# Optimization experiments

Hardware: AMD Instinct MI355X
Metric: run time of the kernel (lower is better)

Reference implementation:

```python
import jax, jax.numpy as jnp
import numpy as np

DIM = 2048   # token width; == heads*head_dim
H, DH = 16, 128
B, S = 1, 2048
E, K = 4, 2          # routed experts, top-k
HID = 5632           # per-expert SwiGLU hidden: round256(int(2*(4*DIM)/3))
HS = 2816            # shared expert hidden: round256(int(2*(2*DIM)/3))


def setup_inputs() -> dict:
    key = jax.random.key(0)
    ks = jax.random.split(key, 24)
    def g(i, shape, s=0.02):
        return jax.random.normal(ks[i], shape, dtype=jnp.float32) * s
    return {
        "image_tokens": jax.random.normal(ks[0], (B, S, DIM), dtype=jnp.float32),
        "adaln_input": jax.random.normal(ks[1], (B, DIM), dtype=jnp.float32),
        "W_ada": g(2, (DIM, 6 * DIM)), "b_ada": g(3, (6 * DIM,)),
        "Wq": g(4, (DIM, DIM)), "bq": g(5, (DIM,)),
        "Wk": g(6, (DIM, DIM)), "bk": g(7, (DIM,)),
        "Wv": g(8, (DIM, DIM)), "bv": g(9, (DIM,)),
        "q_rms_w": jnp.ones((DIM,), jnp.float32) + g(10, (DIM,)),
        "k_rms_w": jnp.ones((DIM,), jnp.float32) + g(11, (DIM,)),
        "Wo": g(12, (DIM, DIM)), "bo": g(13, (DIM,)),
        "gate_w": g(14, (E, DIM)),
        "We1": g(15, (E, DIM, HID)), "We3": g(16, (E, DIM, HID)), "We2": g(17, (E, HID, DIM)),
        "Ws1": g(18, (DIM, HS)), "Ws3": g(19, (DIM, HS)), "Ws2": g(20, (HS, DIM)),
    }


def _ln(x):  # LayerNorm, elementwise_affine=False, eps=1e-6
    m = jnp.mean(x, -1, keepdims=True)
    v = jnp.var(x, -1, keepdims=True)
    return (x - m) * jax.lax.rsqrt(v + 1e-6)


def _rms(x, w):  # RMSNorm with affine weight, eps=1e-5
    return x * jax.lax.rsqrt(jnp.mean(x * x, -1, keepdims=True) + 1e-5) * w


def reference(image_tokens, adaln_input, W_ada, b_ada, Wq, bq, Wk, bk, Wv, bv,
              q_rms_w, k_rms_w, Wo, bo, gate_w, We1, We3, We2, Ws1, Ws3, Ws2):
    # adaLN: SiLU -> Linear -> 6 chunks, each broadcast as [B,1,dim]
    mod = (jax.nn.silu(adaln_input) @ W_ada + b_ada)[:, None, :]
    sh_msa, sc_msa, g_msa, sh_mlp, sc_mlp, g_mlp = jnp.split(mod, 6, axis=-1)

    # attention branch
    x = _ln(image_tokens) * (1.0 + sc_msa) + sh_msa
    q = _rms(x @ Wq + bq, q_rms_w).reshape(B, S, H, DH)
    k = _rms(x @ Wk + bk, k_rms_w).reshape(B, S, H, DH)
    v = (x @ Wv + bv).reshape(B, S, H, DH)
    att = jax.nn.softmax(jnp.einsum('bihd,bjhd->bhij', q, k) / jnp.sqrt(jnp.float32(DH)), axis=-1)
    o = jnp.einsum('bhij,bjhd->bihd', att, v).reshape(B, S, DIM) @ Wo + bo
    img = g_msa * o + image_tokens

    # MoE SwiGLU FFN branch
    y = _ln(img) * (1.0 + sc_mlp) + sh_mlp
    xf = y.reshape(-1, DIM)                                   # [N, dim]
    scores = jax.nn.softmax(xf @ gate_w.T, axis=-1)           # [N, E]
    tw, ti = jax.lax.top_k(scores, K)                         # no top-k renorm (norm_topk_prob=False)
    comb = jnp.zeros((xf.shape[0], E), xf.dtype).at[jnp.arange(xf.shape[0])[:, None], ti].add(tw)
    h = jax.nn.silu(jnp.einsum('nd,edh->neh', xf, We1)) * jnp.einsum('nd,edh->neh', xf, We3)
    routed = jnp.einsum('neh,ehd,ne->nd', h, We2, comb)
    shared = (jax.nn.silu(xf @ Ws1) * (xf @ Ws3)) @ Ws2
    ff = (routed + shared).reshape(B, S, DIM)

    return g_mlp * ff + img
```

## Files before the change

kernel.cpp:

```cpp
#include <hip/hip_runtime.h>
#include <hip/hip_bf16.h>

typedef unsigned short u16;
typedef __bf16 bf16x8 __attribute__((ext_vector_type(8)));
typedef float f32x4 __attribute__((ext_vector_type(4)));
typedef unsigned short u16x8 __attribute__((ext_vector_type(8)));

constexpr int DIMC = 2048;
constexpr int SEQ = 2048;
constexpr int NHEAD = 16;
constexpr int HDIM = 128;
constexpr int NEXP = 4;
constexpr int HIDC = 5632;
constexpr int HSH = 2816;
constexpr int MOD6 = 6 * DIMC;
constexpr int RSTRIDE = 2304;

static __device__ __forceinline__ u16 f2bf(float f) {
  __hip_bfloat16 b = __float2bfloat16(f);
  return __builtin_bit_cast(u16, b);
}
static __device__ __forceinline__ float bf2f(u16 u) {
  unsigned int x = ((unsigned int)u) << 16;
  return __builtin_bit_cast(float, x);
}
static __device__ __forceinline__ float sigf(float x) { return 1.f / (1.f + __expf(-x)); }
static __device__ __forceinline__ void splitf(float f, u16& h, u16& l) {
  h = f2bf(f);
  l = f2bf(f - bf2f(h));
}

static __device__ __forceinline__ void gload16(const void* src, void* dst) {
  __builtin_amdgcn_global_load_lds((const __attribute__((address_space(1))) void*)src,
                                   (__attribute__((address_space(3))) void*)dst, 16, 0, 0);
}

static __device__ __forceinline__ float blockSum(float v) {
#pragma unroll
  for (int m = 1; m < 64; m <<= 1) v += __shfl_xor(v, m);
  __shared__ float s[4];
  int w = threadIdx.x >> 6;
  if ((threadIdx.x & 63) == 0) s[w] = v;
  __syncthreads();
  float r = s[0] + s[1] + s[2] + s[3];
  __syncthreads();
  return r;
}

__global__ __launch_bounds__(256) void k_transpose(const float* __restrict__ in, u16* __restrict__ out,
                                                   int R, int C, int ldin, size_t inz, size_t outz) {
  __shared__ __align__(16) float tile[32][33];
  const float* inp = in + (size_t)blockIdx.z * inz;
  u16* outp = out + (size_t)blockIdx.z * outz;
  int tx = threadIdx.x & 31, ty = threadIdx.x >> 5;
  int c0 = blockIdx.x * 32, r0 = blockIdx.y * 32;
#pragma unroll
  for (int i = 0; i < 32; i += 8)
    tile[ty + i][tx] = inp[(size_t)(r0 + ty + i) * ldin + c0 + tx];
  __syncthreads();
#pragma unroll
  for (int i = 0; i < 32; i += 8)
    outp[(size_t)(c0 + ty + i) * R + r0 + tx] = f2bf(tile[tx][ty + i]);
}

__global__ __launch_bounds__(256) void k_transpose_s(const float* __restrict__ in, u16* __restrict__ outh,
                                                     u16* __restrict__ outl, int R, int C, int ldin) {
  __shared__ __align__(16) float tile[32][33];
  int tx = threadIdx.x & 31, ty = threadIdx.x >> 5;
  int c0 = blockIdx.x * 32, r0 = blockIdx.y * 32;
#pragma unroll
  for (int i = 0; i < 32; i += 8)
    tile[ty + i][tx] = in[(size_t)(r0 + ty + i) * ldin + c0 + tx];
  __syncthreads();
#pragma unroll
  for (int i = 0; i < 32; i += 8) {
    float v = tile[tx][ty + i];
    u16 h, l;
    splitf(v, h, l);
    size_t idx = (size_t)(c0 + ty + i) * R + r0 + tx;
    outh[idx] = h;
    outl[idx] = l;
  }
}

__global__ __launch_bounds__(256) void k_adaln_p(const float* __restrict__ a, const float* __restrict__ W,
                                                 float* __restrict__ partial) {
  __shared__ float sa[128];
  int tid = threadIdx.x, slice = blockIdx.y;
  if (tid < 128) { float v = a[slice * 128 + tid]; sa[tid] = v * sigf(v); }
  __syncthreads();
  int j = blockIdx.x * 256 + tid;
  float acc = 0.f;
#pragma unroll 4
  for (int d = 0; d < 128; ++d) acc += sa[d] * W[(size_t)(slice * 128 + d) * MOD6 + j];
  partial[(size_t)slice * MOD6 + j] = acc;
}
__global__ __launch_bounds__(256) void k_adaln_r(const float* __restrict__ partial, const float* __restrict__ b,
                                                 float* __restrict__ mod) {
  int j = blockIdx.x * 256 + threadIdx.x;
  float acc = b[j];
#pragma unroll
  for (int s = 0; s < 16; ++s) acc += partial[(size_t)s * MOD6 + j];
  mod[j] = acc;
}

__global__ __launch_bounds__(256) void k_ln_mod_split(const float* __restrict__ X, const float* __restrict__ mod,
                                                      int shOff, int scOff, u16* __restrict__ outh,
                                                      u16* __restrict__ outl) {
  int row = blockIdx.x, tid = threadIdx.x;
  const float4* x4 = (const float4*)(X + (size_t)row * DIMC);
  float4 v0 = x4[tid * 2], v1 = x4[tid * 2 + 1];
  float s = v0.x + v0.y + v0.z + v0.w + v1.x + v1.y + v1.z + v1.w;
  float ss = v0.x * v0.x + v0.y * v0.y + v0.z * v0.z + v0.w * v0.w +
             v1.x * v1.x + v1.y * v1.y + v1.z * v1.z + v1.w * v1.w;
  s = blockSum(s);
  ss = blockSum(ss);
  float mean = s * (1.f / DIMC);
  float var = ss * (1.f / DIMC) - mean * mean;
  float rstd = rsqrtf(var + 1e-6f);
  const float* sh = mod + shOff;
  const float* sc = mod + scOff;
  int c = tid * 8;
  float xv[8] = {v0.x, v0.y, v0.z, v0.w, v1.x, v1.y, v1.z, v1.w};
  u16x8 oh, ol;
#pragma unroll
  for (int e = 0; e < 8; ++e) {
    float v = (xv[e] - mean) * rstd * (1.f + sc[c + e]) + sh[c + e];
    u16 h, l;
    splitf(v, h, l);
    oh[e] = h;
    ol[e] = l;
  }
  *(u16x8*)(outh + (size_t)row * DIMC + c) = oh;
  *(u16x8*)(outl + (size_t)row * DIMC + c) = ol;
}

__global__ __launch_bounds__(256) void k_ln_mod(const float* __restrict__ X, const float* __restrict__ mod,
                                                int shOff, int scOff, u16* __restrict__ out) {
  int row = blockIdx.x, tid = threadIdx.x;
  const float4* x4 = (const float4*)(X + (size_t)row * DIMC);
  float4 v0 = x4[tid * 2], v1 = x4[tid * 2 + 1];
  float s = v0.x + v0.y + v0.z + v0.w + v1.x + v1.y + v1.z + v1.w;
  float ss = v0.x * v0.x + v0.y * v0.y + v0.z * v0.z + v0.w * v0.w +
             v1.x * v1.x + v1.y * v1.y + v1.z * v1.z + v1.w * v1.w;
  s = blockSum(s);
  ss = blockSum(ss);
  float mean = s * (1.f / DIMC);
  float var = ss * (1.f / DIMC) - mean * mean;
  float rstd = rsqrtf(var + 1e-6f);
  const float* sh = mod + shOff;
  const float* sc = mod + scOff;
  int c = tid * 8;
  float xv[8] = {v0.x, v0.y, v0.z, v0.w, v1.x, v1.y, v1.z, v1.w};
  u16x8 o;
#pragma unroll
  for (int e = 0; e < 8; ++e) o[e] = f2bf((xv[e] - mean) * rstd * (1.f + sc[c + e]) + sh[c + e]);
  *(u16x8*)(out + (size_t)row * DIMC + c) = o;
}

__global__ __launch_bounds__(256) void k_rms_split(const float* __restrict__ X, int ldin,
                                                   const float* __restrict__ w, float scale,
                                                   u16* __restrict__ outh, u16* __restrict__ outl) {
  int row = blockIdx.x, tid = threadIdx.x;
  const float4* x4 = (const float4*)(X + (size_t)row * ldin);
  float4 v0 = x4[tid * 2], v1 = x4[tid * 2 + 1];
  float ss = v0.x * v0.x + v0.y * v0.y + v0.z * v0.z + v0.w * v0.w +
             v1.x * v1.x + v1.y * v1.y + v1.z * v1.z + v1.w * v1.w;
  ss = blockSum(ss);
  float rstd = rsqrtf(ss * (1.f / DIMC) + 1e-5f) * scale;
  int c = tid * 8;
  float xv[8] = {v0.x, v0.y, v0.z, v0.w, v1.x, v1.y, v1.z, v1.w};
  u16x8 oh, ol;
#pragma unroll
  for (int e = 0; e < 8; ++e) {
    float v = xv[e] * rstd * w[c + e];
    u16 h, l;
    splitf(v, h, l);
    oh[e] = h;
    ol[e] = l;
  }
  *(u16x8*)(outh + (size_t)row * DIMC + c) = oh;
  *(u16x8*)(outl + (size_t)row * DIMC + c) = ol;
}

__global__ __launch_bounds__(256) void k_gate(const float* __restrict__ img, const float* __restrict__ mod,
                                              const float* __restrict__ gw, float* __restrict__ comb) {
  int n = blockIdx.x, tid = threadIdx.x;
  const float4* x4 = (const float4*)(img + (size_t)n * DIMC);
  float4 v0 = x4[tid * 2], v1 = x4[tid * 2 + 1];
  float s = v0.x + v0.y + v0.z + v0.w + v1.x + v1.y + v1.z + v1.w;
  float ss = v0.x * v0.x + v0.y * v0.y + v0.z * v0.z + v0.w * v0.w +
             v1.x * v1.x + v1.y * v1.y + v1.z * v1.z + v1.w * v1.w;
  s = blockSum(s);
  ss = blockSum(ss);
  float mean = s * (1.f / DIMC);
  float var = ss * (1.f / DIMC) - mean * mean;
  float rstd = rsqrtf(var + 1e-6f);
  const float* sh = mod + 3 * DIMC;
  const float* sc = mod + 4 * DIMC;
  int c = tid * 8;
  float xv[8] = {v0.x, v0.y, v0.z, v0.w, v1.x, v1.y, v1.z, v1.w};
  float y[8];
#pragma unroll
  for (int e = 0; e < 8; ++e) y[e] = (xv[e] - mean) * rstd * (1.f + sc[c + e]) + sh[c + e];
  float accs[NEXP];
#pragma unroll
  for (int ex = 0; ex < NEXP; ++ex) {
    float a = 0.f;
#pragma unroll
    for (int e = 0; e < 8; ++e) a += y[e] * gw[(size_t)ex * DIMC + c + e];
    accs[ex] = blockSum(a);
  }
  if (tid == 0) {
    float mx = fmaxf(fmaxf(accs[0], accs[1]), fmaxf(accs[2], accs[3]));
    float ex0 = __expf(accs[0] - mx), ex1 = __expf(accs[1] - mx);
    float ex2 = __expf(accs[2] - mx), ex3 = __expf(accs[3] - mx);
    float inv = 1.f / (ex0 + ex1 + ex2 + ex3);
    float v[4] = {ex0 * inv, ex1 * inv, ex2 * inv, ex3 * inv};
    int i1 = 0;
    for (int e = 1; e < 4; ++e)
      if (v[e] > v[i1]) i1 = e;
    int i2 = -1;
    for (int e = 0; e < 4; ++e) {
      if (e == i1) continue;
      if (i2 < 0 || v[e] > v[i2]) i2 = e;
    }
    for (int e = 0; e < 4; ++e) comb[(size_t)n * 4 + e] = (e == i1 || e == i2) ? v[e] : 0.f;
  }
}

__global__ __launch_bounds__(256) void k_route(const float* __restrict__ comb, int* __restrict__ gidx,
                                               float* __restrict__ cw, int* __restrict__ Mpad) {
  int wid = threadIdx.x >> 6, lane = threadIdx.x & 63;
  int base = 0;
  for (int c = 0; c < SEQ; c += 64) {
    int n = c + lane;
    float w = comb[(size_t)n * NEXP + wid];
    bool sel = w > 0.f;
    unsigned long long mask = __ballot(sel);
    int pos = __popcll(mask & ((1ull << lane) - 1ull));
    if (sel) {
      gidx[wid * RSTRIDE + base + pos] = n;
      cw[wid * RSTRIDE + base + pos] = w;
    }
    base += __popcll(mask);
  }
  int padded = (base + 127) & ~127;
  for (int i = base + lane; i < padded; i += 64) {
    gidx[wid * RSTRIDE + i] = -1;
    cw[wid * RSTRIDE + i] = 0.f;
  }
  if (lane == 0) Mpad[wid] = padded;
}

__global__ __launch_bounds__(256, 2) void k_gemmD(const u16* __restrict__ A, const u16* __restrict__ BT,
                                                  int M, int N, int K, float* __restrict__ Cf) {
  __shared__ __align__(16) u16 As[2][8192], Bs[2][8192];
  const int tid = threadIdx.x, wid = tid >> 6, lane = tid & 63;
  const int l16 = lane & 15, g = lane >> 4;
  const int wr = wid >> 1, wc = wid & 1;
  const int m0 = blockIdx.y * 128, n0 = blockIdx.x * 128;
  const int srow = lane >> 2, scol = (lane & 3) * 8;
  const u16* aS0 = A + (size_t)(m0 + wid * 32 + srow) * K + scol;
  const u16* aS1 = aS0 + (size_t)16 * K;
  const u16* bS0 = BT + (size_t)(n0 + wid * 32 + srow) * K + scol;
  const u16* bS1 = bS0 + (size_t)16 * K;

  const f32x4 zero4 = {0.f, 0.f, 0.f, 0.f};
  f32x4 acc[4][4];
#pragma unroll
  for (int mi = 0; mi < 4; ++mi)
#pragma unroll
    for (int ni = 0; ni < 4; ++ni) acc[mi][ni] = zero4;

  auto stage = [&](int b, int k0) {
    gload16(aS0 + k0, &As[b][wid * 1024]);
    gload16(aS1 + k0, &As[b][wid * 1024 + 512]);
    gload16(aS0 + k0 + 32, &As[b][4096 + wid * 1024]);
    gload16(aS1 + k0 + 32, &As[b][4096 + wid * 1024 + 512]);
    gload16(bS0 + k0, &Bs[b][wid * 1024]);
    gload16(bS1 + k0, &Bs[b][wid * 1024 + 512]);
    gload16(bS0 + k0 + 32, &Bs[b][4096 + wid * 1024]);
    gload16(bS1 + k0 + 32, &Bs[b][4096 + wid * 1024 + 512]);
  };
  auto compute = [&](int b) {
#pragma unroll
    for (int hh = 0; hh < 2; ++hh) {
      const u16* Asrc = &As[b][hh * 4096];
      const u16* Bsrc = &Bs[b][hh * 4096];
      bf16x8 af[4], bfr[4];
#pragma unroll
      for (int mi = 0; mi < 4; ++mi)
        af[mi] = *(const bf16x8*)(&Asrc[(wr * 64 + mi * 16 + l16) * 32 + g * 8]);
#pragma unroll
      for (int ni = 0; ni < 4; ++ni)
        bfr[ni] = *(const bf16x8*)(&Bsrc[(wc * 64 + ni * 16 + l16) * 32 + g * 8]);
#pragma unroll
      for (int mi = 0; mi < 4; ++mi)
#pragma unroll
        for (int ni = 0; ni < 4; ++ni)
          acc[mi][ni] = __builtin_amdgcn_mfma_f32_16x16x32_bf16(af[mi], bfr[ni], acc[mi][ni], 0, 0, 0);
    }
  };

  stage(0, 0);
  __syncthreads();
  for (int k0 = 0; k0 < K; k0 += 128) {
    if (k0 + 64 < K) stage(1, k0 + 64);
    compute(0);
    __syncthreads();
    if (k0 + 128 < K) stage(0, k0 + 128);
    compute(1);
    __syncthreads();
  }

#pragma unroll
  for (int mi = 0; mi < 4; ++mi)
#pragma unroll
    for (int ni = 0; ni < 4; ++ni) {
      const int col = n0 + wc * 64 + ni * 16 + l16;
#pragma unroll
      for (int r = 0; r < 4; ++r) {
        const int row = m0 + wr * 64 + mi * 16 + g * 4 + r;
        Cf[(size_t)row * N + col] = acc[mi][ni][r];
      }
    }
}

template <int GATH>
__global__ __launch_bounds__(256, 2) void k_gemmUP(const u16* __restrict__ A, const u16* __restrict__ B1T0,
                                                   const u16* __restrict__ B3T0, size_t bz, int N, int K,
                                                   const int* __restrict__ gidx0,
                                                   const float* __restrict__ cw0,
                                                   const int* __restrict__ Mp0, u16* __restrict__ G0,
                                                   size_t cz) {
  const int z = blockIdx.z;
  const int m0 = blockIdx.y * 128;
  const int* gidxE = nullptr;
  const float* cwE = nullptr;
  if constexpr (GATH) {
    if (m0 >= Mp0[z]) return;
    gidxE = gidx0 + (size_t)z * RSTRIDE;
    cwE = cw0 + (size_t)z * RSTRIDE;
  }
  const u16* B1T = B1T0 + (size_t)z * bz;
  const u16* B3T = B3T0 + (size_t)z * bz;
  u16* G = G0 + (size_t)z * cz;

  __shared__ __align__(16) u16 As[8192], B1s[8192], B3s[8192];
  const int tid = threadIdx.x, wid = tid >> 6, lane = tid & 63;
  const int l16 = lane & 15, g = lane >> 4;
  const int wr = wid >> 1, wc = wid & 1;
  const int n0 = blockIdx.x * 128;
  const int srow = lane >> 2, scol = (lane & 3) * 8;
  const int slot0 = m0 + wid * 32 + srow;
  int row0, row1;
  if constexpr (GATH) {
    int t0 = gidxE[slot0], t1 = gidxE[slot0 + 16];
    row0 = t0 < 0 ? 0 : t0;
    row1 = t1 < 0 ? 0 : t1;
  } else {
    row0 = slot0;
    row1 = slot0 + 16;
  }
  const u16* aS0 = A + (size_t)row0 * K + scol;
  const u16* aS1 = A + (size_t)row1 * K + scol;
  const u16* b1S0 = B1T + (size_t)(n0 + wid * 32 + srow) * K + scol;
  const u16* b1S1 = b1S0 + (size_t)16 * K;
  const u16* b3S0 = B3T + (size_t)(n0 + wid * 32 + srow) * K + scol;
  const u16* b3S1 = b3S0 + (size_t)16 * K;

  const f32x4 zero4 = {0.f, 0.f, 0.f, 0.f};
  f32x4 acc1[4][4], acc3[4][4];
#pragma unroll
  for (int mi = 0; mi < 4; ++mi)
#pragma unroll
    for (int ni = 0; ni < 4; ++ni) {
      acc1[mi][ni] = zero4;
      acc3[mi][ni] = zero4;
    }

  for (int k0 = 0; k0 < K; k0 += 64) {
    __syncthreads();
    gload16(aS0 + k0, &As[wid * 1024]);
    gload16(aS1 + k0, &As[wid * 1024 + 512]);
    gload16(aS0 + k0 + 32, &As[4096 + wid * 1024]);
    gload16(aS1 + k0 + 32, &As[4096 + wid * 1024 + 512]);
    gload16(b1S0 + k0, &B1s[wid * 1024]);
    gload16(b1S1 + k0, &B1s[wid * 1024 + 512]);
    gload16(b1S0 + k0 + 32, &B1s[4096 + wid * 1024]);
    gload16(b1S1 + k0 + 32, &B1s[4096 + wid * 1024 + 512]);
    gload16(b3S0 + k0, &B3s[wid * 1024]);
    gload16(b3S1 + k0, &B3s[wid * 1024 + 512]);
    gload16(b3S0 + k0 + 32, &B3s[4096 + wid * 1024]);
    gload16(b3S1 + k0 + 32, &B3s[4096 + wid * 1024 + 512]);
    __syncthreads();
#pragma unroll
    for (int hh = 0; hh < 2; ++hh) {
      const u16* Asrc = &As[hh * 4096];
      const u16* B1src = &B1s[hh * 4096];
      const u16* B3src = &B3s[hh * 4096];
      bf16x8 af[4], b1f[4], b3f[4];
#pragma unroll
      for (int mi = 0; mi < 4; ++mi)
        af[mi] = *(const bf16x8*)(&Asrc[(wr * 64 + mi * 16 + l16) * 32 + g * 8]);
#pragma unroll
      for (int ni = 0; ni < 4; ++ni) {
        b1f[ni] = *(const bf16x8*)(&B1src[(wc * 64 + ni * 16 + l16) * 32 + g * 8]);
        b3f[ni] = *(const bf16x8*)(&B3src[(wc * 64 + ni * 16 + l16) * 32 + g * 8]);
      }
#pragma unroll
      for (int mi = 0; mi < 4; ++mi)
#pragma unroll
        for (int ni = 0; ni < 4; ++ni) {
          acc1[mi][ni] = __builtin_amdgcn_mfma_f32_16x16x32_bf16(af[mi], b1f[ni], acc1[mi][ni], 0, 0, 0);
          acc3[mi][ni] = __builtin_amdgcn_mfma_f32_16x16x32_bf16(af[mi], b3f[ni], acc3[mi][ni], 0, 0, 0);
        }
    }
  }

#pragma unroll
  for (int mi = 0; mi < 4; ++mi)
#pragma unroll
    for (int ni = 0; ni < 4; ++ni) {
      const int col = n0 + wc * 64 + ni * 16 + l16;
#pragma unroll
      for (int r = 0; r < 4; ++r) {
        const int slot = m0 + wr * 64 + mi * 16 + g * 4 + r;
        float hv = bf2f(f2bf(acc1[mi][ni][r]));
        float sw = hv * sigf(hv);
        float val = sw * acc3[mi][ni][r];
        if constexpr (GATH) val = val * cwE[slot];
        G[(size_t)slot * N + col] = f2bf(val);
      }
    }
}

__global__ __launch_bounds__(256, 2) void k_gemmR2(const u16* __restrict__ A, const u16* __restrict__ BT,
                                                   int N, int K, const int* __restrict__ gidxE,
                                                   const int* __restrict__ MpE, float* __restrict__ ff) {
  const int m0 = blockIdx.y * 128;
  if (m0 >= *MpE) return;
  __shared__ __align__(16) u16 As[2][8192], Bs[2][8192];
  const int tid = threadIdx.x, wid = tid >> 6, lane = tid & 63;
  const int l16 = lane & 15, g = lane >> 4;
  const int wr = wid >> 1, wc = wid & 1;
  const int n0 = blockIdx.x * 128;
  const int srow = lane >> 2, scol = (lane & 3) * 8;
  const int slot0 = m0 + wid * 32 + srow;
  const u16* aS0 = A + (size_t)slot0 * K + scol;
  const u16* aS1 = A + (size_t)(slot0 + 16) * K + scol;
  const u16* bS0 = BT + (size_t)(n0 + wid * 32 + srow) * K + scol;
  const u16* bS1 = bS0 + (size_t)16 * K;

  const f32x4 zero4 = {0.f, 0.f, 0.f, 0.f};
  f32x4 acc[4][4];
#pragma unroll
  for (int mi = 0; mi < 4; ++mi)
#pragma unroll
    for (int ni = 0; ni < 4; ++ni) acc[mi][ni] = zero4;

  auto stage = [&](int b, int k0) {
    gload16(aS0 + k0, &As[b][wid * 1024]);
    gload16(aS1 + k0, &As[b][wid * 1024 + 512]);
    gload16(aS0 + k0 + 32, &As[b][4096 + wid * 1024]);
    gload16(aS1 + k0 + 32, &As[b][4096 + wid * 1024 + 512]);
    gload16(bS0 + k0, &Bs[b][wid * 1024]);
    gload16(bS1 + k0, &Bs[b][wid * 1024 + 512]);
    gload16(bS0 + k0 + 32, &Bs[b][4096 + wid * 1024]);
    gload16(bS1 + k0 + 32, &Bs[b][4096 + wid * 1024 + 512]);
  };
  auto compute = [&](int b) {
#pragma unroll
    for (int hh = 0; hh < 2; ++hh) {
      const u16* Asrc = &As[b][hh * 4096];
      const u16* Bsrc = &Bs[b][hh * 4096];
      bf16x8 af[4], bfr[4];
#pragma unroll
      for (int mi = 0; mi < 4; ++mi)
        af[mi] = *(const bf16x8*)(&Asrc[(wr * 64 + mi * 16 + l16) * 32 + g * 8]);
#pragma unroll
      for (int ni = 0; ni < 4; ++ni)
        bfr[ni] = *(const bf16x8*)(&Bsrc[(wc * 64 + ni * 16 + l16) * 32 + g * 8]);
#pragma unroll
      for (int mi = 0; mi < 4; ++mi)
#pragma unroll
        for (int ni = 0; ni < 4; ++ni)
          acc[mi][ni] = __builtin_amdgcn_mfma_f32_16x16x32_bf16(af[mi], bfr[ni], acc[mi][ni], 0, 0, 0);
    }
  };

  stage(0, 0);
  __syncthreads();
  for (int k0 = 0; k0 < K; k0 += 128) {
    if (k0 + 64 < K) stage(1, k0 + 64);
    compute(0);
    __syncthreads();
    if (k0 + 128 < K) stage(0, k0 + 128);
    compute(1);
    __syncthreads();
  }

#pragma unroll
  for (int mi = 0; mi < 4; ++mi)
#pragma unroll
    for (int ni = 0; ni < 4; ++ni) {
      const int col = n0 + wc * 64 + ni * 16 + l16;
#pragma unroll
      for (int r = 0; r < 4; ++r) {
        const int slot = m0 + wr * 64 + mi * 16 + g * 4 + r;
        int t = gidxE[slot];
        if (t >= 0) ff[(size_t)t * N + col] += acc[mi][ni][r];
      }
    }
}

template <int MODE>
__global__ __launch_bounds__(256, 2) void k_gemm3s(const u16* __restrict__ Ahg, const u16* __restrict__ Alg,
                                                   const u16* __restrict__ Bhg, const u16* __restrict__ Blg,
                                                   int M, int N, int K, float* __restrict__ Cf,
                                                   const float* __restrict__ bias0,
                                                   const float* __restrict__ bias1,
                                                   const float* __restrict__ bias2,
                                                   const float* __restrict__ gvec,
                                                   const float* __restrict__ resid) {
  __shared__ __align__(16) u16 Ahs[2][4096], Als[2][4096], Bhs[2][4096], Bls[2][4096];
  const int tid = threadIdx.x, wid = tid >> 6, lane = tid & 63;
  const int l16 = lane & 15, g = lane >> 4;
  const int wr = wid >> 1, wc = wid & 1;
  const int m0 = blockIdx.y * 128, n0 = blockIdx.x * 128;
  const int srow = lane >> 2, scol = (lane & 3) * 8;
  const size_t aOff0 = (size_t)(m0 + wid * 32 + srow) * K + scol;
  const size_t aOff1 = aOff0 + (size_t)16 * K;
  const size_t bOff0 = (size_t)(n0 + wid * 32 + srow) * K + scol;
  const size_t bOff1 = bOff0 + (size_t)16 * K;

  const f32x4 zero4 = {0.f, 0.f, 0.f, 0.f};
  f32x4 acc[4][4];
#pragma unroll
  for (int mi = 0; mi < 4; ++mi)
#pragma unroll
    for (int ni = 0; ni < 4; ++ni) acc[mi][ni] = zero4;

  auto stage = [&](int b, int k0) {
    gload16(Ahg + aOff0 + k0, &Ahs[b][wid * 1024]);
    gload16(Ahg + aOff1 + k0, &Ahs[b][wid * 1024 + 512]);
    gload16(Alg + aOff0 + k0, &Als[b][wid * 1024]);
    gload16(Alg + aOff1 + k0, &Als[b][wid * 1024 + 512]);
    gload16(Bhg + bOff0 + k0, &Bhs[b][wid * 1024]);
    gload16(Bhg + bOff1 + k0, &Bhs[b][wid * 1024 + 512]);
    gload16(Blg + bOff0 + k0, &Bls[b][wid * 1024]);
    gload16(Blg + bOff1 + k0, &Bls[b][wid * 1024 + 512]);
  };
  auto compute = [&](int b) {
    bf16x8 bhf[4], blf[4];
#pragma unroll
    for (int ni = 0; ni < 4; ++ni) {
      bhf[ni] = *(const bf16x8*)(&Bhs[b][(wc * 64 + ni * 16 + l16) * 32 + g * 8]);
      blf[ni] = *(const bf16x8*)(&Bls[b][(wc * 64 + ni * 16 + l16) * 32 + g * 8]);
    }
#pragma unroll
    for (int mi = 0; mi < 4; ++mi) {
      bf16x8 ahf = *(const bf16x8*)(&Ahs[b][(wr * 64 + mi * 16 + l16) * 32 + g * 8]);
      bf16x8 alf = *(const bf16x8*)(&Als[b][(wr * 64 + mi * 16 + l16) * 32 + g * 8]);
#pragma unroll
      for (int ni = 0; ni < 4; ++ni) {
        acc[mi][ni] = __builtin_amdgcn_mfma_f32_16x16x32_bf16(alf, bhf[ni], acc[mi][ni], 0, 0, 0);
        acc[mi][ni] = __builtin_amdgcn_mfma_f32_16x16x32_bf16(ahf, blf[ni], acc[mi][ni], 0, 0, 0);
        acc[mi][ni] = __builtin_amdgcn_mfma_f32_16x16x32_bf16(ahf, bhf[ni], acc[mi][ni], 0, 0, 0);
      }
    }
  };

  stage(0, 0);
  __syncthreads();
  for (int k0 = 0; k0 < K; k0 += 64) {
    if (k0 + 32 < K) stage(1, k0 + 32);
    compute(0);
    __syncthreads();
    if (k0 + 64 < K) stage(0, k0 + 64);
    compute(1);
    __syncthreads();
  }

  const float* bp = bias0;
  if constexpr (MODE == 7) bp = (n0 < DIMC) ? bias0 : (n0 < 2 * DIMC ? bias1 : bias2);
#pragma unroll
  for (int mi = 0; mi < 4; ++mi)
#pragma unroll
    for (int ni = 0; ni < 4; ++ni) {
      const int col = n0 + wc * 64 + ni * 16 + l16;
      float bv = bp ? bp[col & (DIMC - 1)] : 0.f;
#pragma unroll
      for (int r = 0; r < 4; ++r) {
        const int row = m0 + wr * 64 + mi * 16 + g * 4 + r;
        float v = acc[mi][ni][r] + bv;
        if constexpr (MODE == 7) {
          Cf[(size_t)row * N + col] = v;
        } else {
          Cf[(size_t)row * N + col] = v * gvec[col] + resid[(size_t)row * N + col];
        }
      }
    }
}

__global__ __launch_bounds__(256, 3) void k_flash3(const u16* __restrict__ qh_g, const u16* __restrict__ ql_g,
                                                   const u16* __restrict__ kh_g, const u16* __restrict__ kl_g,
                                                   const u16* __restrict__ vth_g, const u16* __restrict__ vtl_g,
                                                   u16* __restrict__ oh_g, u16* __restrict__ ol_g) {
  __shared__ __align__(16) u16 Kh[4096], Kl[4096], Vh[128 * 40], Vl[128 * 40];
  __shared__ __align__(16) u16 Pah[4][16 * 40], Pal[4][16 * 40];
  const int tid = threadIdx.x, wid = tid >> 6, lane = tid & 63;
  const int l16 = lane & 15, g = lane >> 4;
  const int h = blockIdx.y;
  const int r0 = blockIdx.x * 64 + wid * 16;
  const size_t hOff = (size_t)h * HDIM;

  bf16x8 qfh[4], qfl[4];
#pragma unroll
  for (int kc = 0; kc < 4; ++kc) {
    const size_t qo = (size_t)(r0 + l16) * DIMC + hOff + kc * 32 + g * 8;
    qfh[kc] = *(const bf16x8*)(qh_g + qo);
    qfl[kc] = *(const bf16x8*)(ql_g + qo);
  }

  const int kr = tid >> 3, ke0 = (tid & 7) * 16;
  const int kswz = (kr & 7) << 4;
  const int kc0 = (ke0 * 2) ^ kswz, kc1 = (ke0 * 2 + 16) ^ kswz;
  char* khp = (char*)Kh + kr * 256;
  char* klp = (char*)Kl + kr * 256;
  const size_t kOff = (size_t)kr * DIMC + hOff + ke0;
  const int vr = tid >> 1, ve0 = (tid & 1) * 16;
  char* vhp = (char*)Vh + vr * 80 + ve0 * 2;
  char* vlp = (char*)Vl + vr * 80 + ve0 * 2;
  const size_t vOff = (size_t)(hOff + vr) * SEQ + ve0;

  u16x8 kH0, kH1, kL0, kL1, vH0, vH1, vL0, vL1;
  kH0 = *(const u16x8*)(kh_g + kOff);
  kH1 = *(const u16x8*)(kh_g + kOff + 8);
  kL0 = *(const u16x8*)(kl_g + kOff);
  kL1 = *(const u16x8*)(kl_g + kOff + 8);
  vH0 = *(const u16x8*)(vth_g + vOff);
  vH1 = *(const u16x8*)(vth_g + vOff + 8);
  vL0 = *(const u16x8*)(vtl_g + vOff);
  vL1 = *(const u16x8*)(vtl_g + vOff + 8);

  const f32x4 zero4 = {0.f, 0.f, 0.f, 0.f};
  f32x4 oacc[8];
#pragma unroll
  for (int db = 0; db < 8; ++db) oacc[db] = zero4;
  float mr[4], lr[4];
#pragma unroll
  for (int r = 0; r < 4; ++r) {
    mr[r] = -3.0e38f;
    lr[r] = 0.f;
  }

  for (int j0 = 0; j0 < SEQ; j0 += 32) {
    __syncthreads();
    *(u16x8*)(khp + kc0) = kH0;
    *(u16x8*)(khp + kc1) = kH1;
    *(u16x8*)(klp + kc0) = kL0;
    *(u16x8*)(klp + kc1) = kL1;
    *(u16x8*)(vhp) = vH0;
    *(u16x8*)(vhp + 16) = vH1;
    *(u16x8*)(vlp) = vL0;
    *(u16x8*)(vlp + 16) = vL1;
    __syncthreads();
    if (j0 + 32 < SEQ) {
      const size_t ko = kOff + (size_t)(j0 + 32) * DIMC;
      const size_t vo = vOff + j0 + 32;
      kH0 = *(const u16x8*)(kh_g + ko);
      kH1 = *(const u16x8*)(kh_g + ko + 8);
      kL0 = *(const u16x8*)(kl_g + ko);
      kL1 = *(const u16x8*)(kl_g + ko + 8);
      vH0 = *(const u16x8*)(vth_g + vo);
      vH1 = *(const u16x8*)(vth_g + vo + 8);
      vL0 = *(const u16x8*)(vtl_g + vo);
      vL1 = *(const u16x8*)(vtl_g + vo + 8);
    }
    f32x4 s0 = zero4, s1 = zero4;
    __builtin_amdgcn_s_setprio(1);
#pragma unroll
    for (int kc = 0; kc < 4; ++kc) {
      const int cb = (kc * 64 + g * 16) ^ ((l16 & 7) << 4);
      bf16x8 kh0 = *(const bf16x8*)((char*)Kh + l16 * 256 + cb);
      bf16x8 kl0 = *(const bf16x8*)((char*)Kl + l16 * 256 + cb);
      bf16x8 kh1 = *(const bf16x8*)((char*)Kh + (16 + l16) * 256 + cb);
      bf16x8 kl1 = *(const bf16x8*)((char*)Kl + (16 + l16) * 256 + cb);
      s0 = __builtin_amdgcn_mfma_f32_16x16x32_bf16(qfl[kc], kh0, s0, 0, 0, 0);
      s0 = __builtin_amdgcn_mfma_f32_16x16x32_bf16(qfh[kc], kl0, s0, 0, 0, 0);
      s0 = __builtin_amdgcn_mfma_f32_16x16x32_bf16(qfh[kc], kh0, s0, 0, 0, 0);
      s1 = __builtin_amdgcn_mfma_f32_16x16x32_bf16(qfl[kc], kh1, s1, 0, 0, 0);
      s1 = __builtin_amdgcn_mfma_f32_16x16x32_bf16(qfh[kc], kl1, s1, 0, 0, 0);
      s1 = __builtin_amdgcn_mfma_f32_16x16x32_bf16(qfh[kc], kh1, s1, 0, 0, 0);
    }
    __builtin_amdgcn_s_setprio(0);
    float corr[4];
#pragma unroll
    for (int r = 0; r < 4; ++r) {
      float tm = fmaxf(s0[r], s1[r]);
#pragma unroll
      for (int m = 1; m < 16; m <<= 1) tm = fmaxf(tm, __shfl_xor(tm, m));
      float mn = fmaxf(mr[r], tm);
      corr[r] = __expf(mr[r] - mn);
      mr[r] = mn;
      float p0 = __expf(s0[r] - mn);
      float p1 = __expf(s1[r] - mn);
      lr[r] = lr[r] * corr[r] + p0 + p1;
      u16 p0h = f2bf(p0), p1h = f2bf(p1);
      Pah[wid][(g * 4 + r) * 40 + l16] = p0h;
      Pah[wid][(g * 4 + r) * 40 + 16 + l16] = p1h;
      Pal[wid][(g * 4 + r) * 40 + l16] = f2bf(p0 - bf2f(p0h));
      Pal[wid][(g * 4 + r) * 40 + 16 + l16] = f2bf(p1 - bf2f(p1h));
    }
#pragma unroll
    for (int db = 0; db < 8; ++db)
#pragma unroll
      for (int r = 0; r < 4; ++r) oacc[db][r] *= corr[r];
    bf16x8 pfh = *(const bf16x8*)(&Pah[wid][l16 * 40 + g * 8]);
    bf16x8 pfl = *(const bf16x8*)(&Pal[wid][l16 * 40 + g * 8]);
    __builtin_amdgcn_s_setprio(1);
#pragma unroll
    for (int db = 0; db < 8; ++db) {
      const int row = db * 16 + l16;
      bf16x8 vh = *(const bf16x8*)((char*)Vh + row * 80 + g * 16);
      bf16x8 vl = *(const bf16x8*)((char*)Vl + row * 80 + g * 16);
      oacc[db] = __builtin_amdgcn_mfma_f32_16x16x32_bf16(pfl, vh, oacc[db], 0, 0, 0);
      oacc[db] = __builtin_amdgcn_mfma_f32_16x16x32_bf16(pfh, vl, oacc[db], 0, 0, 0);
      oacc[db] = __builtin_amdgcn_mfma_f32_16x16x32_bf16(pfh, vh, oacc[db], 0, 0, 0);
    }
    __builtin_amdgcn_s_setprio(0);
  }
#pragma unroll
  for (int r = 0; r < 4; ++r) {
#pragma unroll
    for (int m = 1; m < 16; m <<= 1) lr[r] += __shfl_xor(lr[r], m);
    lr[r] = 1.f / lr[r];
  }
#pragma unroll
  for (int db = 0; db < 8; ++db)
#pragma unroll
    for (int r = 0; r < 4; ++r) {
      float v = oacc[db][r] * lr[r];
      u16 hh, ll;
      splitf(v, hh, ll);
      const size_t idx = (size_t)(r0 + g * 4 + r) * DIMC + hOff + db * 16 + l16;
      oh_g[idx] = hh;
      ol_g[idx] = ll;
    }
}

__global__ __launch_bounds__(256) void k_final(const float* __restrict__ ff, const float* img,
                                               const float* __restrict__ mod, float* out) {
  const float4* gm = (const float4*)(mod + 5 * DIMC);
  const int total = SEQ * DIMC / 4;
  const int stride = gridDim.x * blockDim.x;
  for (int i = blockIdx.x * blockDim.x + threadIdx.x; i < total; i += stride) {
    int col4 = i & (DIMC / 4 - 1);
    float4 gv = gm[col4];
    float4 fv = ((const float4*)ff)[i];
    float4 iv = ((const float4*)img)[i];
    float4 ov;
    ov.x = gv.x * fv.x + iv.x;
    ov.y = gv.y * fv.y + iv.y;
    ov.z = gv.z * fv.z + iv.z;
    ov.w = gv.w * fv.w + iv.w;
    ((float4*)out)[i] = ov;
  }
}

extern "C" void kernel_launch(void* const* d_in, const int* in_sizes, int n_in, void* d_out, int out_size,
                              void* d_ws, size_t ws_size, hipStream_t stream) {
  (void)in_sizes; (void)n_in; (void)out_size; (void)ws_size;
  const float* image_tokens = (const float*)d_in[0];
  const float* adaln_input = (const float*)d_in[1];
  const float* W_ada = (const float*)d_in[2];
  const float* b_ada = (const float*)d_in[3];
  const float* Wq = (const float*)d_in[4];
  const float* bq = (const float*)d_in[5];
  const float* Wk = (const float*)d_in[6];
  const float* bk = (const float*)d_in[7];
  const float* Wv = (const float*)d_in[8];
  const float* bv = (const float*)d_in[9];
  const float* q_rms_w = (const float*)d_in[10];
  const float* k_rms_w = (const float*)d_in[11];
  const float* Wo = (const float*)d_in[12];
  const float* bo = (const float*)d_in[13];
  const float* gate_w = (const float*)d_in[14];
  const float* We1 = (const float*)d_in[15];
  const float* We3 = (const float*)d_in[16];
  const float* We2 = (const float*)d_in[17];
  const float* Ws1 = (const float*)d_in[18];
  const float* Ws3 = (const float*)d_in[19];
  const float* Ws2 = (const float*)d_in[20];

  char* cur = (char*)d_ws;
  auto alloc = [&](size_t n) {
    char* p = cur;
    cur += (n + 255) & ~(size_t)255;
    return p;
  };
  float* modv = (float*)alloc((size_t)MOD6 * 4);
  float* adap = (float*)alloc((size_t)16 * MOD6 * 4);
  float* comb = (float*)alloc((size_t)SEQ * NEXP * 4);
  int* gidx = (int*)alloc((size_t)NEXP * RSTRIDE * 4);
  float* cw = (float*)alloc((size_t)NEXP * RSTRIDE * 4);
  int* Mpad = (int*)alloc((size_t)NEXP * 4);
  u16* xh = (u16*)alloc((size_t)SEQ * DIMC * 2);
  u16* xl = (u16*)alloc((size_t)SEQ * DIMC * 2);
  u16* wTh3 = (u16*)alloc((size_t)3 * DIMC * DIMC * 2);
  u16* wTl3 = (u16*)alloc((size_t)3 * DIMC * DIMC * 2);
  float* tf3 = (float*)alloc((size_t)SEQ * 3 * DIMC * 4);
  u16* qhb = (u16*)alloc((size_t)SEQ * DIMC * 2);
  u16* qlb = (u16*)alloc((size_t)SEQ * DIMC * 2);
  u16* khb = (u16*)alloc((size_t)SEQ * DIMC * 2);
  u16* klb = (u16*)alloc((size_t)SEQ * DIMC * 2);
  u16* vth = (u16*)alloc((size_t)SEQ * DIMC * 2);
  u16* vtl = (u16*)alloc((size_t)SEQ * DIMC * 2);
  u16* aoh = (u16*)alloc((size_t)SEQ * DIMC * 2);
  u16* aol = (u16*)alloc((size_t)SEQ * DIMC * 2);
  u16* x_act = (u16*)alloc((size_t)SEQ * DIMC * 2);
  float* ff = (float*)alloc((size_t)SEQ * DIMC * 4);
  float* img = (float*)d_out;
  const size_t BZ = (size_t)HIDC * DIMC;
  const size_t CZ = (size_t)RSTRIDE * HIDC;
  u16* moe0 = xh;
  u16* wbufE1 = moe0;
  u16* wbufE3 = moe0 + 2 * BZ;
  u16* G2 = moe0 + 4 * BZ;
  u16* wbufS1 = moe0;
  u16* wbufS3 = moe0 + (size_t)HSH * DIMC;
  u16* wbufS2 = moe0 + (size_t)2 * HSH * DIMC;
  u16* Gs = moe0 + (size_t)3 * HSH * DIMC;

  dim3 blk(256);

  k_adaln_p<<<dim3(MOD6 / 256, 16), blk, 0, stream>>>(adaln_input, W_ada, adap);
  k_adaln_r<<<dim3(MOD6 / 256), blk, 0, stream>>>(adap, b_ada, modv);

  k_ln_mod_split<<<dim3(SEQ), blk, 0, stream>>>(image_tokens, modv, 0, DIMC, xh, xl);
  k_transpose_s<<<dim3(DIMC / 32, DIMC / 32), blk, 0, stream>>>(Wq, wTh3, wTl3, DIMC, DIMC, DIMC);
  k_transpose_s<<<dim3(DIMC / 32, DIMC / 32), blk, 0, stream>>>(
      Wk, wTh3 + (size_t)DIMC * DIMC, wTl3 + (size_t)DIMC * DIMC, DIMC, DIMC, DIMC);
  k_transpose_s<<<dim3(DIMC / 32, DIMC / 32), blk, 0, stream>>>(
      Wv, wTh3 + (size_t)2 * DIMC * DIMC, wTl3 + (size_t)2 * DIMC * DIMC, DIMC, DIMC, DIMC);
  k_gemm3s<7><<<dim3(3 * DIMC / 128, SEQ / 128), blk, 0, stream>>>(
      xh, xl, wTh3, wTl3, SEQ, 3 * DIMC, DIMC, tf3, bq, bk, bv, nullptr, nullptr);
  k_rms_split<<<dim3(SEQ), blk, 0, stream>>>(tf3, 3 * DIMC, q_rms_w, 0.08838834764831845f, qhb, qlb);
  k_rms_split<<<dim3(SEQ), blk, 0, stream>>>(tf3 + DIMC, 3 * DIMC, k_rms_w, 1.f, khb, klb);
  k_transpose_s<<<dim3(DIMC / 32, SEQ / 32), blk, 0, stream>>>(tf3 + 2 * DIMC, vth, vtl, SEQ, DIMC,
                                                               3 * DIMC);
  k_flash3<<<dim3(SEQ / 64, NHEAD), blk, 0, stream>>>(qhb, qlb, khb, klb, vth, vtl, aoh, aol);
  k_transpose_s<<<dim3(DIMC / 32, DIMC / 32), blk, 0, stream>>>(Wo, wTh3, wTl3, DIMC, DIMC, DIMC);
  k_gemm3s<2><<<dim3(DIMC / 128, SEQ / 128), blk, 0, stream>>>(
      aoh, aol, wTh3, wTl3, SEQ, DIMC, DIMC, img, bo, nullptr, nullptr, modv + 2 * DIMC, image_tokens);

  k_ln_mod<<<dim3(SEQ), blk, 0, stream>>>(img, modv, 3 * DIMC, 4 * DIMC, x_act);
  k_gate<<<dim3(SEQ), blk, 0, stream>>>(img, modv, gate_w, comb);
  k_route<<<dim3(1), blk, 0, stream>>>(comb, gidx, cw, Mpad);

  k_transpose<<<dim3(HSH / 32, DIMC / 32), blk, 0, stream>>>(Ws1, wbufS1, DIMC, HSH, HSH, 0, 0);
  k_transpose<<<dim3(HSH / 32, DIMC / 32), blk, 0, stream>>>(Ws3, wbufS3, DIMC, HSH, HSH, 0, 0);
  k_gemmUP<0><<<dim3(HSH / 128, SEQ / 128, 1), blk, 0, stream>>>(
      x_act, wbufS1, wbufS3, 0, HSH, DIMC, nullptr, nullptr, nullptr, Gs, 0);
  k_transpose<<<dim3(DIMC / 32, HSH / 32), blk, 0, stream>>>(Ws2, wbufS2, HSH, DIMC, DIMC, 0, 0);
  k_gemmD<<<dim3(DIMC / 128, SEQ / 128), blk, 0, stream>>>(Gs, wbufS2, SEQ, DIMC, HSH, ff);

  const size_t WE = (size_t)DIMC * HIDC;
  for (int p = 0; p < 2; ++p) {
    const int e0 = p * 2;
    k_transpose<<<dim3(HIDC / 32, DIMC / 32, 2), blk, 0, stream>>>(We1 + (size_t)e0 * WE, wbufE1,
                                                                   DIMC, HIDC, HIDC, WE, BZ);
    k_transpose<<<dim3(HIDC / 32, DIMC / 32, 2), blk, 0, stream>>>(We3 + (size_t)e0 * WE, wbufE3,
                                                                   DIMC, HIDC, HIDC, WE, BZ);
    k_gemmUP<1><<<dim3(HIDC / 128, SEQ / 128, 2), blk, 0, stream>>>(
        x_act, wbufE1, wbufE3, BZ, HIDC, DIMC, gidx + e0 * RSTRIDE, cw + e0 * RSTRIDE, Mpad + e0, G2,
        CZ);
    k_transpose<<<dim3(DIMC / 32, HIDC / 32, 2), blk, 0, stream>>>(We2 + (size_t)e0 * WE, wbufE1,
                                                                   HIDC, DIMC, DIMC, WE, BZ);
    for (int z = 0; z < 2; ++z) {
      k_gemmR2<<<dim3(DIMC / 128, SEQ / 128), blk, 0, stream>>>(
          G2 + (size_t)z * CZ, wbufE1 + (size_t)z * BZ, DIMC, HIDC, gidx + (e0 + z) * RSTRIDE,
          Mpad + e0 + z, ff);
    }
  }

  k_final<<<dim3(1024), blk, 0, stream>>>(ff, img, modv, (float*)d_out);
}
```

Measured before the change: 1.541 ms.

## Swizzle workgroups across XCDs and batch expert down-projection into one launch

Adds an XCD-aware block index remap to the GEMM kernels and re-linearises the flash attention grid, so blocks that share operands land on the same XCD and its L2. The two per-expert down-projection GEMMs now run as one z-batched launch. To avoid write conflicts, the second expert accumulates into a separate zeroed buffer, and the final kernel sums both buffers. This adds a memset and an extra buffer read in the final pass in exchange for better cache locality and fuller occupancy.

```diff
diff --git a/kernel.cpp b/kernel.cpp
--- a/kernel.cpp
+++ b/kernel.cpp
@@ -33,6 +33,17 @@
 static __device__ __forceinline__ void gload16(const void* src, void* dst) {
   __builtin_amdgcn_global_load_lds((const __attribute__((address_space(1))) void*)src,
                                    (__attribute__((address_space(3))) void*)dst, 16, 0, 0);
+}
+
+static __device__ __forceinline__ void xcd_swz(int& bx, int& by, int& bz) {
+  const int nx = gridDim.x, ny = gridDim.y;
+  const int flat = blockIdx.x + nx * (blockIdx.y + ny * blockIdx.z);
+  const int nwg = nx * ny * gridDim.z;
+  const int swz = (flat & 7) * (nwg >> 3) + (flat >> 3);
+  bx = swz % nx;
+  const int t = swz / nx;
+  by = t % ny;
+  bz = t / ny;
 }
 
 static __device__ __forceinline__ float blockSum(float v) {
@@ -255,11 +266,13 @@
 
 __global__ __launch_bounds__(256, 2) void k_gemmD(const u16* __restrict__ A, const u16* __restrict__ BT,
                                                   int M, int N, int K, float* __restrict__ Cf) {
+  int bx, by, bzz;
+  xcd_swz(bx, by, bzz);
   __shared__ __align__(16) u16 As[2][8192], Bs[2][8192];
   const int tid = threadIdx.x, wid = tid >> 6, lane = tid & 63;
   const int l16 = lane & 15, g = lane >> 4;
   const int wr = wid >> 1, wc = wid & 1;
-  const int m0 = blockIdx.y * 128, n0 = blockIdx.x * 128;
+  const int m0 = by * 128, n0 = bx * 128;
   const int srow = lane >> 2, scol = (lane & 3) * 8;
   const u16* aS0 = A + (size_t)(m0 + wid * 32 + srow) * K + scol;
   const u16* aS1 = aS0 + (size_t)16 * K;
@@ -329,13 +342,15 @@
 
 template <int GATH>
 __global__ __launch_bounds__(256, 2) void k_gemmUP(const u16* __restrict__ A, const u16* __restrict__ B1T0,
-                                                   const u16* __restrict__ B3T0, size_t bz, int N, int K,
+                                                   const u16* __restrict__ B3T0, size_t bzs, int N, int K,
                                                    const int* __restrict__ gidx0,
                                                    const float* __restrict__ cw0,
                                                    const int* __restrict__ Mp0, u16* __restrict__ G0,
                                                    size_t cz) {
-  const int z = blockIdx.z;
-  const int m0 = blockIdx.y * 128;
+  int bx, by, bz;
+  xcd_swz(bx, by, bz);
+  const int z = bz;
+  const int m0 = by * 128;
   const int* gidxE = nullptr;
   const float* cwE = nullptr;
   if constexpr (GATH) {
@@ -343,15 +358,15 @@
     gidxE = gidx0 + (size_t)z * RSTRIDE;
     cwE = cw0 + (size_t)z * RSTRIDE;
   }
-  const u16* B1T = B1T0 + (size_t)z * bz;
-  const u16* B3T = B3T0 + (size_t)z * bz;
+  const u16* B1T = B1T0 + (size_t)z * bzs;
+  const u16* B3T = B3T0 + (size_t)z * bzs;
   u16* G = G0 + (size_t)z * cz;
 
   __shared__ __align__(16) u16 As[8192], B1s[8192], B3s[8192];
   const int tid = threadIdx.x, wid = tid >> 6, lane = tid & 63;
   const int l16 = lane & 15, g = lane >> 4;
   const int wr = wid >> 1, wc = wid & 1;
-  const int n0 = blockIdx.x * 128;
+  const int n0 = bx * 128;
   const int srow = lane >> 2, scol = (lane & 3) * 8;
   const int slot0 = m0 + wid * 32 + srow;
   int row0, row1;
@@ -436,16 +451,26 @@
     }
 }
 
-__global__ __launch_bounds__(256, 2) void k_gemmR2(const u16* __restrict__ A, const u16* __restrict__ BT,
-                                                   int N, int K, const int* __restrict__ gidxE,
-                                                   const int* __restrict__ MpE, float* __restrict__ ff) {
-  const int m0 = blockIdx.y * 128;
-  if (m0 >= *MpE) return;
+__global__ __launch_bounds__(256, 2) void k_gemmR2(const u16* __restrict__ A0, size_t az,
+                                                   const u16* __restrict__ BT0, size_t bzs, int N, int K,
+                                                   const int* __restrict__ gidx0,
+                                                   const int* __restrict__ Mp0, float* __restrict__ ffA,
+                                                   float* __restrict__ ffB) {
+  int bx, by, bz;
+  xcd_swz(bx, by, bz);
+  const int z = bz;
+  const int m0 = by * 128;
+  if (m0 >= Mp0[z]) return;
+  const int* gidxE = gidx0 + (size_t)z * RSTRIDE;
+  const u16* A = A0 + (size_t)z * az;
+  const u16* BT = BT0 + (size_t)z * bzs;
+  float* ff = z ? ffB : ffA;
+
   __shared__ __align__(16) u16 As[2][8192], Bs[2][8192];
   const int tid = threadIdx.x, wid = tid >> 6, lane = tid & 63;
   const int l16 = lane & 15, g = lane >> 4;
   const int wr = wid >> 1, wc = wid & 1;
-  const int n0 = blockIdx.x * 128;
+  const int n0 = bx * 128;
   const int srow = lane >> 2, scol = (lane & 3) * 8;
   const int slot0 = m0 + wid * 32 + srow;
   const u16* aS0 = A + (size_t)slot0 * K + scol;
@@ -524,11 +549,13 @@
                                                    const float* __restrict__ bias2,
                                                    const float* __restrict__ gvec,
                                                    const float* __restrict__ resid) {
+  int bxs, bys, bzs2;
+  xcd_swz(bxs, bys, bzs2);
   __shared__ __align__(16) u16 Ahs[2][4096], Als[2][4096], Bhs[2][4096], Bls[2][4096];
   const int tid = threadIdx.x, wid = tid >> 6, lane = tid & 63;
   const int l16 = lane & 15, g = lane >> 4;
   const int wr = wid >> 1, wc = wid & 1;
-  const int m0 = blockIdx.y * 128, n0 = blockIdx.x * 128;
+  const int m0 = bys * 128, n0 = bxs * 128;
   const int srow = lane >> 2, scol = (lane & 3) * 8;
   const size_t aOff0 = (size_t)(m0 + wid * 32 + srow) * K + scol;
   const size_t aOff1 = aOff0 + (size_t)16 * K;
@@ -612,8 +639,10 @@
   __shared__ __align__(16) u16 Pah[4][16 * 40], Pal[4][16 * 40];
   const int tid = threadIdx.x, wid = tid >> 6, lane = tid & 63;
   const int l16 = lane & 15, g = lane >> 4;
-  const int h = blockIdx.y;
-  const int r0 = blockIdx.x * 64 + wid * 16;
+  const int bid = blockIdx.x;
+  const int h = (bid & 7) + ((bid >> 8) << 3);
+  const int qb = (bid >> 3) & 31;
+  const int r0 = qb * 64 + wid * 16;
   const size_t hOff = (size_t)h * HDIM;
 
   bf16x8 qfh[4], qfl[4];
@@ -751,21 +780,23 @@
     }
 }
 
-__global__ __launch_bounds__(256) void k_final(const float* __restrict__ ff, const float* img,
-                                               const float* __restrict__ mod, float* out) {
+__global__ __launch_bounds__(256) void k_final(const float* __restrict__ ffA, const float* __restrict__ ffB,
+                                               const float* img, const float* __restrict__ mod,
+                                               float* out) {
   const float4* gm = (const float4*)(mod + 5 * DIMC);
   const int total = SEQ * DIMC / 4;
   const int stride = gridDim.x * blockDim.x;
   for (int i = blockIdx.x * blockDim.x + threadIdx.x; i < total; i += stride) {
     int col4 = i & (DIMC / 4 - 1);
     float4 gv = gm[col4];
-    float4 fv = ((const float4*)ff)[i];
+    float4 fa = ((const float4*)ffA)[i];
+    float4 fb = ((const float4*)ffB)[i];
     float4 iv = ((const float4*)img)[i];
     float4 ov;
-    ov.x = gv.x * fv.x + iv.x;
-    ov.y = gv.y * fv.y + iv.y;
-    ov.z = gv.z * fv.z + iv.z;
-    ov.w = gv.w * fv.w + iv.w;
+    ov.x = gv.x * (fa.x + fb.x) + iv.x;
+    ov.y = gv.y * (fa.y + fb.y) + iv.y;
+    ov.z = gv.z * (fa.z + fb.z) + iv.z;
+    ov.w = gv.w * (fa.w + fb.w) + iv.w;
     ((float4*)out)[i] = ov;
   }
 }
@@ -822,6 +853,7 @@
   u16* aol = (u16*)alloc((size_t)SEQ * DIMC * 2);
   u16* x_act = (u16*)alloc((size_t)SEQ * DIMC * 2);
   float* ff = (float*)alloc((size_t)SEQ * DIMC * 4);
+  float* ffB = (float*)alloc((size_t)SEQ * DIMC * 4);
   float* img = (float*)d_out;
   const size_t BZ = (size_t)HIDC * DIMC;
   const size_t CZ = (size_t)RSTRIDE * HIDC;
@@ -851,7 +883,7 @@
   k_rms_split<<<dim3(SEQ), blk, 0, stream>>>(tf3 + DIMC, 3 * DIMC, k_rms_w, 1.f, khb, klb);
   k_transpose_s<<<dim3(DIMC / 32, SEQ / 32), blk, 0, stream>>>(tf3 + 2 * DIMC, vth, vtl, SEQ, DIMC,
                                                                3 * DIMC);
-  k_flash3<<<dim3(SEQ / 64, NHEAD), blk, 0, stream>>>(qhb, qlb, khb, klb, vth, vtl, aoh, aol);
+  k_flash3<<<dim3(SEQ / 64 * NHEAD), blk, 0, stream>>>(qhb, qlb, khb, klb, vth, vtl, aoh, aol);
   k_transpose_s<<<dim3(DIMC / 32, DIMC / 32), blk, 0, stream>>>(Wo, wTh3, wTl3, DIMC, DIMC, DIMC);
   k_gemm3s<2><<<dim3(DIMC / 128, SEQ / 128), blk, 0, stream>>>(
       aoh, aol, wTh3, wTl3, SEQ, DIMC, DIMC, img, bo, nullptr, nullptr, modv + 2 * DIMC, image_tokens);
@@ -859,6 +891,7 @@
   k_ln_mod<<<dim3(SEQ), blk, 0, stream>>>(img, modv, 3 * DIMC, 4 * DIMC, x_act);
   k_gate<<<dim3(SEQ), blk, 0, stream>>>(img, modv, gate_w, comb);
   k_route<<<dim3(1), blk, 0, stream>>>(comb, gidx, cw, Mpad);
+  hipMemsetAsync(ffB, 0, (size_t)SEQ * DIMC * 4, stream);
 
   k_transpose<<<dim3(HSH / 32, DIMC / 32), blk, 0, stream>>>(Ws1, wbufS1, DIMC, HSH, HSH, 0, 0);
   k_transpose<<<dim3(HSH / 32, DIMC / 32), blk, 0, stream>>>(Ws3, wbufS3, DIMC, HSH, HSH, 0, 0);
@@ -879,12 +912,9 @@
         CZ);
     k_transpose<<<dim3(DIMC / 32, HIDC / 32, 2), blk, 0, stream>>>(We2 + (size_t)e0 * WE, wbufE1,
                                                                    HIDC, DIMC, DIMC, WE, BZ);
-    for (int z = 0; z < 2; ++z) {
-      k_gemmR2<<<dim3(DIMC / 128, SEQ / 128), blk, 0, stream>>>(
-          G2 + (size_t)z * CZ, wbufE1 + (size_t)z * BZ, DIMC, HIDC, gidx + (e0 + z) * RSTRIDE,
-          Mpad + e0 + z, ff);
-    }
-  }
-
-  k_final<<<dim3(1024), blk, 0, stream>>>(ff, img, modv, (float*)d_out);
-}
+    k_gemmR2<<<dim3(DIMC / 128, SEQ / 128, 2), blk, 0, stream>>>(
+        G2, CZ, wbufE1, BZ, DIMC, HIDC, gidx + e0 * RSTRIDE, Mpad + e0, ff, ffB);
+  }
+
+  k_final<<<dim3(1024), blk, 0, stream>>>(ff, ffB, img, modv, (float*)d_out);
+}
```

New measurement: 1.535 ms. No clear change (-0.4%).
